# Performance work log

Measured on AMD Instinct MI355X. Metric: run time of the kernel, lower is better.

## Reference

```python
import jax, jax.numpy as jnp
import numpy as np

TOP_K = 8
N_EXPERTS = 64
HIDDEN = 4096


def setup_inputs() -> dict:
    key = jax.random.key(0)
    k1, k2 = jax.random.split(key)
    hidden_states = jax.random.normal(k1, (4, 4096, HIDDEN), dtype=jnp.float32)
    # kaiming_uniform_(a=sqrt(5)) on a (64, 4096) weight -> U(-b, b), b = sqrt(6/((1+5)*4096)) = 1/sqrt(4096)
    bound = 1.0 / np.sqrt(HIDDEN)
    weight = jax.random.uniform(k2, (N_EXPERTS, HIDDEN), dtype=jnp.float32,
                                minval=-bound, maxval=bound)
    return {"hidden_states": hidden_states, "weight": weight}


def reference(hidden_states, weight):
    bsz, seq_len, h = hidden_states.shape
    x = hidden_states.reshape(-1, h)                       # [T, H]
    logits = jnp.einsum('th,eh->te', x, weight)            # [T, E]
    scores = jax.nn.softmax(logits, axis=-1)
    topk_weight, topk_idx = jax.lax.top_k(scores, TOP_K)   # [T, K]
    denom = jnp.sum(topk_weight, axis=-1, keepdims=True) + 1e-20
    topk_weight = topk_weight / denom
    topk_weight = topk_weight.reshape(bsz, seq_len, TOP_K)
    topk_idx = topk_idx.reshape(bsz, seq_len, TOP_K)
    # training-time aux loss (seq_aux path): histogram of argmax expert * mean prob
    probs = scores                                         # softmax(logits)
    top1 = jnp.argmax(probs, axis=-1)                      # [T]
    counts = jnp.zeros((N_EXPERTS,), dtype=jnp.float32).at[top1].add(1.0)
    route_prob = jnp.mean(probs, axis=0)                   # [E]
    route_frac = counts / jnp.sum(counts)
    aux_loss = jnp.sum(route_prob * route_frac) * N_EXPERTS
    return topk_idx, topk_weight, aux_loss
```

## Files before the change

### kernel.cpp

```cpp
#include <hip/hip_runtime.h>
#include <hip/hip_bf16.h>

#define TOKS 16384
#define HID  4096
#define NEXP 64
#define EPS  1e-4f

#define WS_FLAGCNT  128
#define WS_FLAGLIST 192
#define WS_BPACK    16576

typedef __attribute__((ext_vector_type(8))) short short8_t;
typedef __attribute__((ext_vector_type(4))) float f32x4;

static __device__ __forceinline__ unsigned short f2bf_rn(float x) {
    unsigned u = __builtin_bit_cast(unsigned, x);
    u = (u + 0x7fffu + ((u >> 16) & 1u)) >> 16;
    return (unsigned short)u;
}
static __device__ __forceinline__ float bf2f(unsigned short h) {
    return __builtin_bit_cast(float, (unsigned)h << 16);
}
static __device__ __forceinline__ void gl2lds16(const void* g, void* l) {
    __builtin_amdgcn_global_load_lds(
        (const __attribute__((address_space(1))) unsigned int*)g,
        (__attribute__((address_space(3))) unsigned int*)l, 16, 0, 0);
}

__global__ void moe_prep(const float* __restrict__ W, unsigned short* __restrict__ Bpk,
                         float* __restrict__ wsf) {
    const int idx = blockIdx.x * blockDim.x + threadIdx.x;
    if (idx < 192) wsf[idx] = 0.0f;
    if (idx >= NEXP * HID) return;
    const int n = idx >> 12;
    const int k = idx & 4095;
    const float w = W[idx];
    const unsigned short hi = f2bf_rn(w);
    const unsigned short lo = f2bf_rn(w - bf2f(hi));
    const int kt   = k >> 5;
    const int nt   = n >> 4;
    const int lane = (n & 15) | (((k >> 3) & 3) << 4);
    const int j    = k & 7;
    const int dst  = (((kt << 2) + nt) << 10) + (lane << 3) + j;
    Bpk[dst]       = hi;
    Bpk[dst + 512] = lo;
}

__global__ __launch_bounds__(512, 1)
void moe_fused(const float* __restrict__ X, const unsigned short* __restrict__ Bpk,
               float* __restrict__ out, float* __restrict__ wsf) {
    __shared__ __align__(16) float xbuf[4][64][68];
    __shared__ __align__(16) unsigned short bbuf[4][8192];
    float (*L)[68] = (float (*)[68])&xbuf[0][0][0];

    const int tid  = threadIdx.x;
    const int lane = tid & 63;
    const int w    = tid >> 6;
    const int mt   = w & 3;
    const int nh   = w >> 2;
    const int g    = lane >> 4;
    const int tok0 = blockIdx.x * 64;

    f32x4 acc[2];
    acc[0] = (f32x4){0.f, 0.f, 0.f, 0.f};
    acc[1] = (f32x4){0.f, 0.f, 0.f, 0.f};

    int ldsoff[3]; size_t gxb[3];
    #pragma unroll
    for (int i = 0; i < 3; ++i) {
        int t = w * 3 + i; if (t >= 17) t -= 17;
        const int off = t * 1024 + (lane << 4);
        const int row = off / 272;
        const int rb  = off - row * 272;
        const int col = (rb < 256) ? (rb >> 2) : 0;
        ldsoff[i] = t * 1024;
        gxb[i] = (size_t)(tok0 + row) * HID + col;
    }

    #define STAGE(bf, ss)                                                              \
    {                                                                                  \
        const int k0_ = (ss) << 6;                                                     \
        _Pragma("unroll")                                                              \
        for (int i = 0; i < 3; ++i)                                                    \
            gl2lds16(X + gxb[i] + k0_, (void*)((char*)&xbuf[bf][0][0] + ldsoff[i]));   \
        _Pragma("unroll")                                                              \
        for (int j = 0; j < 2; ++j) {                                                  \
            const int c1k = (w << 1) + j;                                              \
            gl2lds16((const char*)Bpk + ((size_t)(ss) << 14) + (c1k << 10) + (lane << 4), \
                     (void*)((char*)&bbuf[bf][0] + (c1k << 10)));                      \
        }                                                                              \
    }

    STAGE(0, 0);
    STAGE(1, 1);

    const int tr = (mt << 4) + (lane & 15);

    for (int s = 0; s < 64; ++s) {
        const int cur = s & 3;
        {
            const int ss = (s + 2 < 64) ? (s + 2) : 63;
            STAGE((s + 2) & 3, ss);
        }
        asm volatile("s_waitcnt vmcnt(10)" ::: "memory");
        __builtin_amdgcn_s_barrier();
        __builtin_amdgcn_sched_barrier(0);

        const char* ab = (const char*)&xbuf[cur][0][0] + tr * 272;
        const char* bb = (const char*)&bbuf[cur][0];
        #pragma unroll
        for (int ktl = 0; ktl < 2; ++ktl) {
            const int cl = (ktl << 3) + (g << 1);
            const float4 a0 = *(const float4*)(ab + (cl << 4));
            const float4 a1 = *(const float4*)(ab + (cl << 4) + 16);
            const float xv[8] = {a0.x, a0.y, a0.z, a0.w, a1.x, a1.y, a1.z, a1.w};
            short8_t ah, al;
            #pragma unroll
            for (int j = 0; j < 8; ++j) {
                const unsigned u = __builtin_bit_cast(unsigned, xv[j]);
                ah[j] = (short)(u >> 16);
                const float hif = __builtin_bit_cast(float, u & 0xFFFF0000u);
                al[j] = (short)(__builtin_bit_cast(unsigned, xv[j] - hif) >> 16);
            }
            #pragma unroll
            for (int ntl = 0; ntl < 2; ++ntl) {
                const char* bp = bb + (((ktl << 2) + (nh << 1) + ntl) << 11) + (lane << 4);
                const short8_t bh = *(const short8_t*)bp;
                const short8_t bl = *(const short8_t*)(bp + 1024);
                acc[ntl] = __builtin_amdgcn_mfma_f32_16x16x32_bf16(ah, bh, acc[ntl], 0, 0, 0);
                acc[ntl] = __builtin_amdgcn_mfma_f32_16x16x32_bf16(al, bh, acc[ntl], 0, 0, 0);
                acc[ntl] = __builtin_amdgcn_mfma_f32_16x16x32_bf16(ah, bl, acc[ntl], 0, 0, 0);
            }
        }
    }
    asm volatile("s_waitcnt vmcnt(0)" ::: "memory");
    __syncthreads();

    #pragma unroll
    for (int ntl = 0; ntl < 2; ++ntl)
        #pragma unroll
        for (int r = 0; r < 4; ++r)
            L[(mt << 4) + (g << 2) + r][(nh << 5) + (ntl << 4) + (lane & 15)] = acc[ntl][r];
    __syncthreads();

    float* outIdx = out;
    float* outW   = out + TOKS * 8;
    int* flagcnt  = (int*)wsf + WS_FLAGCNT;
    int* flaglist = (int*)wsf + WS_FLAGLIST;

    float rp = 0.f;
    #pragma unroll
    for (int tt = 0; tt < 8; ++tt) {
        const int tl = (w << 3) + tt;
        const float lg = L[tl][lane];

        float v = lg; int idx = lane;
        #pragma unroll
        for (int size = 2; size <= 64; size <<= 1) {
            #pragma unroll
            for (int str = size >> 1; str > 0; str >>= 1) {
                const float ov = __shfl_xor(v, str, 64);
                const int   oi = __shfl_xor(idx, str, 64);
                const bool pb = (ov > v) || (ov == v && oi < idx);
                const bool keepFirst = ((lane & str) == 0) == ((lane & size) == 0);
                if (pb == keepFirst) { v = ov; idx = oi; }
            }
        }

        const float m = __shfl(v, 0, 64);
        const float p = __expf(lg - m);
        float sdenom = p;
        #pragma unroll
        for (int o = 32; o; o >>= 1) sdenom += __shfl_xor(sdenom, o, 64);
        const float inv_s = 1.0f / sdenom;
        rp += p * inv_s;

        const float wkv = __expf(v - m) * inv_s;
        float d8 = (lane < 8) ? wkv : 0.f;
        #pragma unroll
        for (int o = 1; o < 8; o <<= 1) d8 += __shfl_xor(d8, o, 64);
        const float invd = 1.0f / (d8 + 1e-20f);
        const float nv = __shfl_down(v, 1, 64);
        const bool flg = __any(lane < 8 && (v - nv) < EPS);

        const int gtok = tok0 + tl;
        if (lane < 8) {
            outIdx[(size_t)gtok * 8 + lane] = (float)idx;
            outW[(size_t)gtok * 8 + lane]   = wkv * invd;
        }
        if (lane == 0) {
            atomicAdd(&wsf[NEXP + idx], 1.0f);
            if (flg) {
                const int pos = atomicAdd(flagcnt, 1);
                if (pos < TOKS) flaglist[pos] = gtok;
            }
        }
    }
    atomicAdd(&wsf[lane], rp);
    #undef STAGE
}

__global__ __launch_bounds__(256, 2)
void moe_fix(const float* __restrict__ X, const float* __restrict__ W,
             float* __restrict__ out, float* __restrict__ wsf) {
    __shared__ double red[256];
    const int tid = threadIdx.x;
    const int e   = tid & 63;
    const int kc  = tid >> 6;
    const int nf  = min(*((int*)wsf + WS_FLAGCNT), TOKS);
    const int* flaglist = (const int*)wsf + WS_FLAGLIST;
    float* outIdx = out;
    float* outW   = out + TOKS * 8;

    for (int fi = blockIdx.x; fi < nf; fi += gridDim.x) {
        const int tok = flaglist[fi];
        const float* xrow = X + (size_t)tok * HID + kc * 1024;
        const float* wrow = W + (size_t)e  * HID + kc * 1024;
        double part = 0.0;
        for (int j = 0; j < 1024; j += 4) {
            const float4 xv = *(const float4*)(xrow + j);
            const float4 wv = *(const float4*)(wrow + j);
            part = fma((double)xv.x, (double)wv.x, part);
            part = fma((double)xv.y, (double)wv.y, part);
            part = fma((double)xv.z, (double)wv.z, part);
            part = fma((double)xv.w, (double)wv.w, part);
        }
        red[tid] = part;
        __syncthreads();
        if (tid < 64) {
            const double lg = ((red[tid] + red[64 + tid]) + red[128 + tid]) + red[192 + tid];
            const float lgf = (float)lg;
            float m = lgf;
            #pragma unroll
            for (int o = 32; o; o >>= 1) m = fmaxf(m, __shfl_xor(m, o, 64));
            const float p = __expf(lgf - m);
            float s = p;
            #pragma unroll
            for (int o = 32; o; o >>= 1) s += __shfl_xor(s, o, 64);
            const float inv_s = 1.0f / s;

            double v = lg;
            double bw[8]; int ik[8];
            #pragma unroll
            for (int k = 0; k < 8; ++k) {
                double bv = v; int bi = tid;
                #pragma unroll
                for (int o = 32; o; o >>= 1) {
                    const double ov = __shfl_xor(bv, o, 64);
                    const int    oi = __shfl_xor(bi, o, 64);
                    if (ov > bv || (ov == bv && oi < bi)) { bv = ov; bi = oi; }
                }
                bw[k] = bv; ik[k] = bi;
                if (tid == bi) v = -1.0e300;
            }
            float wk[8]; float denom = 1e-20f;
            #pragma unroll
            for (int k = 0; k < 8; ++k) {
                wk[k] = __expf((float)bw[k] - m) * inv_s; denom += wk[k];
            }
            const float invd = 1.0f / denom;
            const size_t base = (size_t)tok * 8;
            const int oldtop = (int)outIdx[base];
            if (tid < 8) {
                outIdx[base + tid] = (float)ik[tid];
                outW[base + tid]   = wk[tid] * invd;
            }
            if (tid == 0 && ik[0] != oldtop) {
                atomicAdd(&wsf[NEXP + oldtop], -1.0f);
                atomicAdd(&wsf[NEXP + ik[0]],  1.0f);
            }
        }
        __syncthreads();
    }
}

__global__ void moe_final(const float* __restrict__ wsf, float* __restrict__ out) {
    const int e = threadIdx.x;
    float v = wsf[e] * wsf[NEXP + e];
    #pragma unroll
    for (int o = 32; o; o >>= 1) v += __shfl_xor(v, o, 64);
    if (e == 0)
        out[2 * TOKS * 8] = v * (64.0f / ((float)TOKS * (float)TOKS));
}

__global__ void moe_init(float* __restrict__ wsf, int n) {
    const int i = blockIdx.x * blockDim.x + threadIdx.x;
    if (i < n) wsf[i] = 0.0f;
}

__global__ void moe_w_cvt(const float* __restrict__ W, double* __restrict__ Wd) {
    const int i = blockIdx.x * blockDim.x + threadIdx.x;
    if (i < NEXP * HID) Wd[i] = (double)W[i];
}

__global__ __launch_bounds__(512, 2)
void moe_mono(const float* __restrict__ X, const double* __restrict__ Wd,
              float* __restrict__ out, float* __restrict__ wsf) {
    __shared__ double xs[64][66];
    __shared__ double L2[64][65];
    const int tid  = threadIdx.x;
    const int lane = tid & 63;
    const int wid  = __builtin_amdgcn_readfirstlane(tid >> 6);
    const int tok0 = blockIdx.x * 64;
    double acc[8] = {0., 0., 0., 0., 0., 0., 0., 0.};
    for (int h0 = 0; h0 < HID; h0 += 64) {
        #pragma unroll
        for (int i = 0; i < 8; ++i) {
            const int li = tid + i * 512;
            xs[li >> 6][li & 63] = (double)X[((size_t)(tok0 + (li >> 6)) << 12) + (h0 + (li & 63))];
        }
        __syncthreads();
        const double* wchunk = Wd + (((size_t)(wid << 3)) << 12) + h0;
        #pragma unroll 2
        for (int hh = 0; hh < 64; hh += 2) {
            const double2 xv = *(const double2*)&xs[lane][hh];
            #pragma unroll
            for (int e = 0; e < 8; ++e) {
                const double* wr = wchunk + (((size_t)e) << 12) + hh;
                acc[e] = fma(xv.x, wr[0], acc[e]);
                acc[e] = fma(xv.y, wr[1], acc[e]);
            }
        }
        __syncthreads();
    }
    #pragma unroll
    for (int e = 0; e < 8; ++e) L2[lane][(wid << 3) + e] = acc[e];
    __syncthreads();
    float* outIdx = out;
    float* outW   = out + (TOKS * 8);
    float rp = 0.0f;
    for (int tt = 0; tt < 8; ++tt) {
        const int t = (wid << 3) + tt;
        const double lg = L2[t][lane];
        const float lgf = (float)lg;
        float m = lgf;
        #pragma unroll
        for (int o = 32; o; o >>= 1) m = fmaxf(m, __shfl_xor(m, o, 64));
        const float p = __expf(lgf - m);
        float s = p;
        #pragma unroll
        for (int o = 32; o; o >>= 1) s += __shfl_xor(s, o, 64);
        const float inv_s = 1.0f / s;
        rp += p * inv_s;
        double v = lg;
        float wk[8]; int ik[8];
        #pragma unroll
        for (int k = 0; k < 8; ++k) {
            double bv = v; int bi = lane;
            #pragma unroll
            for (int o = 32; o; o >>= 1) {
                const double ov = __shfl_xor(bv, o, 64);
                const int    oi = __shfl_xor(bi, o, 64);
                if (ov > bv || (ov == bv && oi < bi)) { bv = ov; bi = oi; }
            }
            wk[k] = __expf((float)bv - m) * inv_s; ik[k] = bi;
            if (lane == bi) v = -1.0e300;
        }
        if (lane == 0) {
            const float denom = (((wk[0]+wk[1])+(wk[2]+wk[3])) +
                                 ((wk[4]+wk[5])+(wk[6]+wk[7]))) + 1e-20f;
            const float invd = 1.0f / denom;
            const size_t base = ((size_t)(tok0 + t)) << 3;
            #pragma unroll
            for (int k = 0; k < 8; ++k) {
                outIdx[base + k] = (float)ik[k];
                outW[base + k]   = wk[k] * invd;
            }
            atomicAdd(&wsf[NEXP + ik[0]], 1.0f);
        }
    }
    atomicAdd(&wsf[lane], rp);
}

extern "C" void kernel_launch(void* const* d_in, const int* in_sizes, int n_in,
                              void* d_out, int out_size, void* d_ws, size_t ws_size,
                              hipStream_t stream) {
    const float* X = (const float*)d_in[0];
    const float* W = (const float*)d_in[1];
    float* out = (float*)d_out;
    float* wsf = (float*)d_ws;

    const size_t need = 4ull * WS_BPACK + 2ull * 524288;

    if (ws_size >= need) {
        unsigned short* Bpk = (unsigned short*)(wsf + WS_BPACK);
        moe_prep<<<(NEXP * HID + 255) / 256, 256, 0, stream>>>(W, Bpk, wsf);
        moe_fused<<<TOKS / 64, 512, 0, stream>>>(X, Bpk, out, wsf);
        moe_fix<<<256, 256, 0, stream>>>(X, W, out, wsf);
        moe_final<<<1, 64, 0, stream>>>(wsf, out);
    } else {
        double* Wd = (double*)d_ws;
        float* wsf2 = (float*)(Wd + NEXP * HID);
        moe_w_cvt<<<(NEXP * HID + 255) / 256, 256, 0, stream>>>(W, Wd);
        moe_init<<<1, 256, 0, stream>>>(wsf2, 128);
        moe_mono<<<TOKS / 64, 512, 0, stream>>>(X, Wd, out, wsf2);
        moe_final<<<1, 64, 0, stream>>>(wsf2, out);
    }
}
```

Measured before the change: 210.6 us.

## Halve token tile to 32 with 256-thread blocks and double-buffered staging

```diff
diff --git a/kernel.cpp b/kernel.cpp
--- a/kernel.cpp
+++ b/kernel.cpp
@@ -46,35 +46,36 @@
     Bpk[dst + 512] = lo;
 }
 
-__global__ __launch_bounds__(512, 1)
+__global__ __launch_bounds__(256, 2)
 void moe_fused(const float* __restrict__ X, const unsigned short* __restrict__ Bpk,
                float* __restrict__ out, float* __restrict__ wsf) {
-    __shared__ __align__(16) float xbuf[4][64][68];
-    __shared__ __align__(16) unsigned short bbuf[4][8192];
-    float (*L)[68] = (float (*)[68])&xbuf[0][0][0];
+    __shared__ __align__(16) char xraw[2][9216];
+    __shared__ __align__(16) unsigned short bs[2][8192];
+    float (*L)[68] = (float (*)[68])&xraw[0][0];
 
     const int tid  = threadIdx.x;
     const int lane = tid & 63;
     const int w    = tid >> 6;
-    const int mt   = w & 3;
-    const int nh   = w >> 2;
+    const int mt   = w & 1;
+    const int nh   = w >> 1;
     const int g    = lane >> 4;
-    const int tok0 = blockIdx.x * 64;
+    const int tok0 = blockIdx.x * 32;
 
     f32x4 acc[2];
     acc[0] = (f32x4){0.f, 0.f, 0.f, 0.f};
     acc[1] = (f32x4){0.f, 0.f, 0.f, 0.f};
 
-    int ldsoff[3]; size_t gxb[3];
+    int xlds[3]; size_t xsrc[3];
     #pragma unroll
     for (int i = 0; i < 3; ++i) {
-        int t = w * 3 + i; if (t >= 17) t -= 17;
-        const int off = t * 1024 + (lane << 4);
-        const int row = off / 272;
-        const int rb  = off - row * 272;
-        const int col = (rb < 256) ? (rb >> 2) : 0;
-        ldsoff[i] = t * 1024;
-        gxb[i] = (size_t)(tok0 + row) * HID + col;
+        int t = w + 4 * i; if (t > 8) t = w;
+        const int byte  = t * 1024 + (lane << 4);
+        int row = byte / 272;
+        const int inrow = byte - row * 272;
+        int col = (inrow < 256) ? (inrow >> 2) : 0;
+        if (row > 31) { row = 31; col = 0; }
+        xlds[i] = t * 1024;
+        xsrc[i] = (size_t)(tok0 + row) * HID + col;
     }
 
     #define STAGE(bf, ss)                                                              \
@@ -82,37 +83,31 @@
         const int k0_ = (ss) << 6;                                                     \
         _Pragma("unroll")                                                              \
         for (int i = 0; i < 3; ++i)                                                    \
-            gl2lds16(X + gxb[i] + k0_, (void*)((char*)&xbuf[bf][0][0] + ldsoff[i]));   \
+            gl2lds16(X + xsrc[i] + k0_, (void*)(&xraw[bf][0] + xlds[i]));              \
         _Pragma("unroll")                                                              \
-        for (int j = 0; j < 2; ++j) {                                                  \
-            const int c1k = (w << 1) + j;                                              \
-            gl2lds16((const char*)Bpk + ((size_t)(ss) << 14) + (c1k << 10) + (lane << 4), \
-                     (void*)((char*)&bbuf[bf][0] + (c1k << 10)));                      \
+        for (int j = 0; j < 4; ++j) {                                                  \
+            const int t = (w << 2) + j;                                                \
+            gl2lds16((const char*)Bpk + ((size_t)(ss) << 14) + (t << 10) + (lane << 4), \
+                     (void*)((char*)&bs[bf][0] + (t << 10)));                          \
         }                                                                              \
     }
 
     STAGE(0, 0);
-    STAGE(1, 1);
+    asm volatile("s_waitcnt vmcnt(0)" ::: "memory");
+    __syncthreads();
 
     const int tr = (mt << 4) + (lane & 15);
+    int cur = 0;
 
     for (int s = 0; s < 64; ++s) {
-        const int cur = s & 3;
-        {
-            const int ss = (s + 2 < 64) ? (s + 2) : 63;
-            STAGE((s + 2) & 3, ss);
-        }
-        asm volatile("s_waitcnt vmcnt(10)" ::: "memory");
-        __builtin_amdgcn_s_barrier();
-        __builtin_amdgcn_sched_barrier(0);
-
-        const char* ab = (const char*)&xbuf[cur][0][0] + tr * 272;
-        const char* bb = (const char*)&bbuf[cur][0];
+        if (s < 63) STAGE(cur ^ 1, s + 1);
+
+        const char* ab = &xraw[cur][0] + tr * 272;
+        const char* bb = (const char*)&bs[cur][0];
         #pragma unroll
         for (int ktl = 0; ktl < 2; ++ktl) {
-            const int cl = (ktl << 3) + (g << 1);
-            const float4 a0 = *(const float4*)(ab + (cl << 4));
-            const float4 a1 = *(const float4*)(ab + (cl << 4) + 16);
+            const float4 a0 = *(const float4*)(ab + ktl * 128 + g * 32);
+            const float4 a1 = *(const float4*)(ab + ktl * 128 + g * 32 + 16);
             const float xv[8] = {a0.x, a0.y, a0.z, a0.w, a1.x, a1.y, a1.z, a1.w};
             short8_t ah, al;
             #pragma unroll
@@ -132,9 +127,9 @@
                 acc[ntl] = __builtin_amdgcn_mfma_f32_16x16x32_bf16(ah, bl, acc[ntl], 0, 0, 0);
             }
         }
-    }
-    asm volatile("s_waitcnt vmcnt(0)" ::: "memory");
-    __syncthreads();
+        __syncthreads();
+        cur ^= 1;
+    }
 
     #pragma unroll
     for (int ntl = 0; ntl < 2; ++ntl)
@@ -385,7 +380,7 @@
     if (ws_size >= need) {
         unsigned short* Bpk = (unsigned short*)(wsf + WS_BPACK);
         moe_prep<<<(NEXP * HID + 255) / 256, 256, 0, stream>>>(W, Bpk, wsf);
-        moe_fused<<<TOKS / 64, 512, 0, stream>>>(X, Bpk, out, wsf);
+        moe_fused<<<TOKS / 32, 256, 0, stream>>>(X, Bpk, out, wsf);
         moe_fix<<<256, 256, 0, stream>>>(X, W, out, wsf);
         moe_final<<<1, 64, 0, stream>>>(wsf, out);
     } else {
```

New measurement: 239.9 us. 1.14x slower.
